# Optimization experiments

Measured on AMD Instinct MI355X. Metric: run time of the kernel, lower is better.

## Reference

```python
import jax, jax.numpy as jnp
import numpy as np
from jax import lax

EPS = 1e-5
K = 3  # DCN kernel size


def _conv(x, w, pad, lhs_dil=(1, 1)):
    return lax.conv_general_dilated(
        x, w, window_strides=(1, 1), padding=((pad, pad), (pad, pad)),
        lhs_dilation=lhs_dil, dimension_numbers=('NCHW', 'OIHW', 'NCHW'))


def _batchnorm(x, gamma, beta):
    # training-mode BN (batch statistics), matching nn.BatchNorm2d in train()
    m = jnp.mean(x, axis=(0, 2, 3), keepdims=True)
    v = jnp.var(x, axis=(0, 2, 3), keepdims=True)
    return (x - m) * lax.rsqrt(v + EPS) * gamma[None, :, None, None] + beta[None, :, None, None]


def _bilinear_sample(x, py, px):
    # x: [B,C,H,W]; py,px: [B,K2,H,W] fractional sample coords (zero-pad outside)
    B, C, H, W = x.shape
    K2 = py.shape[1]
    y0 = jnp.floor(py)
    x0 = jnp.floor(px)
    wy = (py - y0)[:, None]  # [B,1,K2,H,W]
    wx = (px - x0)[:, None]
    xf = x.reshape(B, C, H * W)

    def gather(yi, xi):
        valid = ((yi >= 0) & (yi <= H - 1) & (xi >= 0) & (xi <= W - 1)).astype(x.dtype)
        yc = jnp.clip(yi, 0, H - 1).astype(jnp.int32)
        xc = jnp.clip(xi, 0, W - 1).astype(jnp.int32)
        idx = (yc * W + xc).reshape(B, 1, -1)
        v = jnp.take_along_axis(xf, idx, axis=2).reshape(B, C, K2, H, W)
        return v * valid[:, None]

    v00 = gather(y0, x0)
    v01 = gather(y0, x0 + 1)
    v10 = gather(y0 + 1, x0)
    v11 = gather(y0 + 1, x0 + 1)
    return (v00 * (1 - wy) * (1 - wx) + v01 * (1 - wy) * wx
            + v10 * wy * (1 - wx) + v11 * wy * wx)  # [B,C,K2,H,W]


def _dcn(x, w_off, b_off, w_dcn, b_dcn):
    # Modulated deformable conv (DCNv2), stride 1, pad 1, dil 1, 1 deform group
    B, C, H, W = x.shape
    K2 = K * K
    om = _conv(x, w_off, pad=1) + b_off[None, :, None, None]  # [B,3*K2,H,W]
    dy, dx, m = om[:, :K2], om[:, K2:2 * K2], jax.nn.sigmoid(om[:, 2 * K2:])
    ki, kj = jnp.meshgrid(jnp.arange(K), jnp.arange(K), indexing='ij')
    ky = (ki.reshape(-1) - 1).astype(x.dtype)[None, :, None, None]
    kx = (kj.reshape(-1) - 1).astype(x.dtype)[None, :, None, None]
    py = dy + jnp.arange(H, dtype=x.dtype)[None, None, :, None] + ky
    px = dx + jnp.arange(W, dtype=x.dtype)[None, None, None, :] + kx
    val = _bilinear_sample(x, py, px) * m[:, None]  # [B,C,K2,H,W]
    Co = w_dcn.shape[0]
    out = jnp.einsum('bikhw,oik->bohw', val, w_dcn.reshape(Co, C, K2))
    return out + b_dcn[None, :, None, None]


def _conv_transpose(x, w_up):
    # torch ConvTranspose2d(k=4, stride=2, pad=1), weight [Cin, Cout, 4, 4]
    w = jnp.flip(w_up, axis=(2, 3)).transpose(1, 0, 2, 3)  # -> OIHW
    return _conv(x, w, pad=2, lhs_dil=(2, 2))


def setup_inputs() -> dict:
    key = jax.random.key(0)
    ks = jax.random.split(key, 8)
    B, Cin, Cout, H, W = 4, 256, 256, 64, 64
    x = jax.random.normal(ks[0], (B, Cin, H, W), dtype=jnp.float32)
    w_off = jax.random.normal(ks[1], (3 * K * K, Cin, K, K), dtype=jnp.float32) * 0.01
    b_off = jnp.zeros((3 * K * K,), dtype=jnp.float32)
    w_dcn = jax.random.normal(ks[2], (Cout, Cin, K, K), dtype=jnp.float32) * (1.0 / np.sqrt(Cin * K * K))
    b_dcn = jnp.zeros((Cout,), dtype=jnp.float32)
    gamma1 = jax.random.uniform(ks[3], (Cout,), dtype=jnp.float32, minval=0.5, maxval=1.5)
    beta1 = jax.random.normal(ks[4], (Cout,), dtype=jnp.float32) * 0.1
    w_up = jax.random.normal(ks[5], (Cout, Cout, 4, 4), dtype=jnp.float32) * (1.0 / np.sqrt(Cout * 16))
    gamma2 = jax.random.uniform(ks[6], (Cout,), dtype=jnp.float32, minval=0.5, maxval=1.5)
    beta2 = jax.random.normal(ks[7], (Cout,), dtype=jnp.float32) * 0.1
    return {'x': x, 'w_off': w_off, 'b_off': b_off, 'w_dcn': w_dcn, 'b_dcn': b_dcn,
            'gamma1': gamma1, 'beta1': beta1, 'w_up': w_up, 'gamma2': gamma2, 'beta2': beta2}


def reference(x, w_off, b_off, w_dcn, b_dcn, gamma1, beta1, w_up, gamma2, beta2):
    out = _dcn(x, w_off, b_off, w_dcn, b_dcn)
    out = jax.nn.relu(_batchnorm(out, gamma1, beta1))
    out = _conv_transpose(out, w_up)
    out = jax.nn.relu(_batchnorm(out, gamma2, beta2))
    return out
```

## Files before the change

### kernel.cpp

```cpp
#include <hip/hip_runtime.h>
#include <hip/hip_bf16.h>
#include <math.h>

#define B_   4
#define CIN  256
#define COUT 256
#define HW   4096

typedef __attribute__((ext_vector_type(8))) short short8;
typedef __attribute__((ext_vector_type(4))) float float4v;

#define LSTR  40
#define LSTR2 72

__device__ __forceinline__ float sigmoidf_(float v){ return 1.0f/(1.0f+expf(-v)); }
__device__ __forceinline__ ushort f2bf(float f){
  union { float f; unsigned u; } x; x.f = f;
  unsigned r = x.u + 0x7fffu + ((x.u>>16)&1u);
  return (ushort)(r>>16);
}
__device__ __forceinline__ float bflo(unsigned u){ union{unsigned u; float f;} c; c.u = u<<16;          return c.f; }
__device__ __forceinline__ float bfhi(unsigned u){ union{unsigned u; float f;} c; c.u = u & 0xffff0000u; return c.f; }

__global__ void k_transpose_x(const float* __restrict__ x, ushort* __restrict__ xtb){
  __shared__ float ts[32][33];
  int tx = threadIdx.x & 31, ty = threadIdx.x >> 5;
  int p0 = blockIdx.x * 32, c0 = blockIdx.y * 32, b = blockIdx.z;
  const float* xb = x + (size_t)b*CIN*HW;
#pragma unroll
  for(int q=0;q<4;q++){
    int c = ty + q*8;
    ts[c][tx] = xb[(size_t)(c0+c)*HW + p0+tx];
  }
  __syncthreads();
#pragma unroll
  for(int q=0;q<4;q++){
    int pr = ty + q*8;
    xtb[((size_t)(b*HW + p0+pr)<<8) + c0+tx] = f2bf(ts[tx][pr]);
  }
}

__global__ void k_build_Wob(const float* __restrict__ w_off, ushort* __restrict__ Wob){
  int f = blockIdx.x*256 + threadIdx.x;
  int kc = f>>10, o = (f>>5)&31, kk = f&31;
  int k = kc*32 + kk, tap = k>>8, c = k&255;
  float v = (o < 27) ? w_off[(size_t)o*2304 + c*9 + tap] : 0.f;
  Wob[f] = f2bf(v);
}
__global__ void k_build_Wdb(const float* __restrict__ w_dcn, ushort* __restrict__ Wdb){
  int f = blockIdx.x*256 + threadIdx.x;
  int kc = f>>13, o = (f>>5)&255, kk = f&31;
  int k = kc>>3, c = ((kc&7)<<5) | kk;
  Wdb[f] = f2bf(w_dcn[(size_t)o*2304 + c*9 + k]);
}
__global__ void k_build_WT2c(const float* __restrict__ w_up, ushort* __restrict__ WT2c){
  int f = blockIdx.x*256 + threadIdx.x;
  int pp = f>>18, kc = (f>>13)&31, o = (f>>5)&255, kk = f&31;
  int k = kc*32 + kk, ab = k>>8, c = k&255;
  int a = ab>>1, bb = ab&1, ph = pp>>1, pw = pp&1;
  WT2c[f] = f2bf(w_up[(size_t)(c*COUT+o)*16 + (3-ph-2*a)*4 + (3-pw-2*bb)]);
}

__global__ __launch_bounds__(256) void k_offset_mfma(const ushort* __restrict__ xtb,
                        const ushort* __restrict__ Wob, float* __restrict__ om){
  __shared__ ushort Vs[2][64*LSTR2];
  __shared__ int sIdx[576];
  int tid = threadIdx.x;
  int px0 = blockIdx.x * 64;
  int b   = blockIdx.y;
  for(int t=tid; t<576; t+=256){
    int tap = t>>6, px = t&63;
    int p = px0+px, hh = p>>6, ww = p&63;
    int ih = hh + tap/3 - 1, iw = ww + tap%3 - 1;
    sIdx[t] = (ih>=0 && ih<64 && iw>=0 && iw<64) ? ((b*HW + ih*64+iw)<<8) : -1;
  }
  __syncthreads();

  int lane = tid&63, wv = tid>>6, lo = lane&15, hi = lane>>4;
  float4v acc[2];
  acc[0] = acc[1] = (float4v){0.f,0.f,0.f,0.f};
  int vpx = tid>>2, vseg = tid&3;
  const int wlane = lo*32 + hi*8;

#define OFF_GATHER_P(PAIR, V0, V1) do{ \
    int k_ = (PAIR)>>2, c0_ = ((PAIR)&3)<<6; \
    int idx_ = sIdx[(k_<<6)+vpx]; \
    int coff_ = c0_ + (vseg<<4); \
    V0 = make_uint4(0,0,0,0); V1 = make_uint4(0,0,0,0); \
    if(idx_ >= 0){ \
      V0 = *(const uint4*)(xtb + idx_ + coff_); \
      V1 = *(const uint4*)(xtb + idx_ + coff_ + 8); \
    } \
  }while(0)

#define OFF_VWRITE_P(V0, V1, BUF) do{ \
    *(uint4*)(&Vs[BUF][vpx*LSTR2 + (vseg<<4)])     = V0; \
    *(uint4*)(&Vs[BUF][vpx*LSTR2 + (vseg<<4) + 8]) = V1; \
  }while(0)

#define OFF_WLOAD_P(PAIR, W) do{ \
    const ushort* wp_ = Wob + (((PAIR)*2)<<10) + wlane; \
    W[0] = *(const short8*)(wp_);        W[1] = *(const short8*)(wp_ + 512); \
    W[2] = *(const short8*)(wp_ + 1024); W[3] = *(const short8*)(wp_ + 1536); \
  }while(0)

#define OFF_COMPUTE_P(W, BUF) do{ \
    const ushort* bp_ = &Vs[BUF][(wv*16+lo)*LSTR2 + hi*8]; \
    short8 ba_ = *(const short8*)(bp_); \
    short8 bb_ = *(const short8*)(bp_ + 32); \
    acc[0] = __builtin_amdgcn_mfma_f32_16x16x32_bf16(W[0], ba_, acc[0], 0,0,0); \
    acc[1] = __builtin_amdgcn_mfma_f32_16x16x32_bf16(W[1], ba_, acc[1], 0,0,0); \
    acc[0] = __builtin_amdgcn_mfma_f32_16x16x32_bf16(W[2], bb_, acc[0], 0,0,0); \
    acc[1] = __builtin_amdgcn_mfma_f32_16x16x32_bf16(W[3], bb_, acc[1], 0,0,0); \
  }while(0)

  short8 wA[4], wB[4];
  uint4 vE0, vE1, vO0, vO1;
  OFF_WLOAD_P(0, wA);
  OFF_GATHER_P(0, vE0, vE1);
  OFF_VWRITE_P(vE0, vE1, 0);
  OFF_GATHER_P(1, vO0, vO1);
  __syncthreads();

#pragma unroll 1
  for(int pb=0; pb<36; pb+=2){
    {
      if(pb<34) OFF_GATHER_P(pb+2, vE0, vE1);
      OFF_WLOAD_P(pb+1, wB);
      OFF_COMPUTE_P(wA, 0);
      OFF_VWRITE_P(vO0, vO1, 1);
      __syncthreads();
    }
    {
      if(pb<33) OFF_GATHER_P(pb+3, vO0, vO1);
      if(pb<34) OFF_WLOAD_P(pb+2, wA);
      OFF_COMPUTE_P(wB, 1);
      if(pb<34) OFF_VWRITE_P(vE0, vE1, 0);
      __syncthreads();
    }
  }
  int p = px0 + wv*16 + lo;
#pragma unroll
  for(int mi=0;mi<2;mi++){
    int ob = mi*16 + hi*4;
    float4v a = (mi==0) ? acc[0] : acc[1];
#pragma unroll
    for(int r=0;r<4;r++){
      int o = ob + r;
      if(o < 27) om[(size_t)(b*27+o)*HW + p] = a[r];
    }
  }
}

#define DCN_GATHER_P(PAIR, C0,C1,C2,C3, CF) do{ \
    int k_ = (PAIR)>>2, c0_ = ((PAIR)&3)<<6; \
    int t_ = (k_<<6) + vpx; \
    int pk_ = sPk[t_]; CF = sCf[t_]; \
    int coff_ = c0_ + (vseg<<3); \
    int iy0_=pk_&63, iy1_=(pk_>>6)&63, ix0_=(pk_>>12)&63, ix1_=(pk_>>18)&63; \
    C0 = *(const uint4*)(xtb + cbase + (((iy0_<<6)+ix0_)<<8) + coff_); \
    C1 = *(const uint4*)(xtb + cbase + (((iy0_<<6)+ix1_)<<8) + coff_); \
    C2 = *(const uint4*)(xtb + cbase + (((iy1_<<6)+ix0_)<<8) + coff_); \
    C3 = *(const uint4*)(xtb + cbase + (((iy1_<<6)+ix1_)<<8) + coff_); \
  }while(0)

#define DCN_BLEND_P(C0,C1,C2,C3, CF, BUF) do{ \
    union{ ushort us[8]; uint4 q; } rr_; \
    rr_.us[0] = f2bf(CF.x*bflo(C0.x)+CF.y*bflo(C1.x)+CF.z*bflo(C2.x)+CF.w*bflo(C3.x)); \
    rr_.us[1] = f2bf(CF.x*bfhi(C0.x)+CF.y*bfhi(C1.x)+CF.z*bfhi(C2.x)+CF.w*bfhi(C3.x)); \
    rr_.us[2] = f2bf(CF.x*bflo(C0.y)+CF.y*bflo(C1.y)+CF.z*bflo(C2.y)+CF.w*bflo(C3.y)); \
    rr_.us[3] = f2bf(CF.x*bfhi(C0.y)+CF.y*bfhi(C1.y)+CF.z*bfhi(C2.y)+CF.w*bfhi(C3.y)); \
    rr_.us[4] = f2bf(CF.x*bflo(C0.z)+CF.y*bflo(C1.z)+CF.z*bflo(C2.z)+CF.w*bflo(C3.z)); \
    rr_.us[5] = f2bf(CF.x*bfhi(C0.z)+CF.y*bfhi(C1.z)+CF.z*bfhi(C2.z)+CF.w*bfhi(C3.z)); \
    rr_.us[6] = f2bf(CF.x*bflo(C0.w)+CF.y*bflo(C1.w)+CF.z*bflo(C2.w)+CF.w*bflo(C3.w)); \
    rr_.us[7] = f2bf(CF.x*bfhi(C0.w)+CF.y*bfhi(C1.w)+CF.z*bfhi(C2.w)+CF.w*bfhi(C3.w)); \
    *(uint4*)(&Vs[BUF][vpx*LSTR2 + (vseg<<3)]) = rr_.q; \
  }while(0)

#define DCN_WLOAD_P(PAIR, W) do{ \
    const ushort* wp_ = Wdb + ((size_t)((PAIR)*2)<<13) + wlane; \
    W[0] = *(const short8*)(wp_);         W[1] = *(const short8*)(wp_ + 512); \
    W[2] = *(const short8*)(wp_ + 1024);  W[3] = *(const short8*)(wp_ + 1536); \
    W[4] = *(const short8*)(wp_ + 8192);  W[5] = *(const short8*)(wp_ + 8704); \
    W[6] = *(const short8*)(wp_ + 9216);  W[7] = *(const short8*)(wp_ + 9728); \
  }while(0)

#define DCN_COMPUTE_P(W, BUF) do{ \
    const ushort* bp_ = &Vs[BUF][(pn0+lo)*LSTR2 + hi*8]; \
    short8 a0_ = *(const short8*)(bp_); \
    short8 a1_ = *(const short8*)(bp_ + 16*LSTR2); \
    short8 b0_ = *(const short8*)(bp_ + 32); \
    short8 b1_ = *(const short8*)(bp_ + 32 + 16*LSTR2); \
    _Pragma("unroll") \
    for(int i_=0;i_<4;i_++){ \
      acc[i_][0] = __builtin_amdgcn_mfma_f32_16x16x32_bf16(W[i_],   a0_, acc[i_][0], 0,0,0); \
      acc[i_][1] = __builtin_amdgcn_mfma_f32_16x16x32_bf16(W[i_],   a1_, acc[i_][1], 0,0,0); \
      acc[i_][0] = __builtin_amdgcn_mfma_f32_16x16x32_bf16(W[4+i_], b0_, acc[i_][0], 0,0,0); \
      acc[i_][1] = __builtin_amdgcn_mfma_f32_16x16x32_bf16(W[4+i_], b1_, acc[i_][1], 0,0,0); \
    } \
  }while(0)

__global__ __launch_bounds__(512) void k_dcn_mfma(const ushort* __restrict__ xtb,
                        const float* __restrict__ om, const float* __restrict__ b_off,
                        const ushort* __restrict__ Wdb, float* __restrict__ out1){
  __shared__ ushort Vs[2][64*LSTR2];
  __shared__ int    sPk[576];
  __shared__ float4 sCf[576];
  int tid = threadIdx.x;
  int px0 = blockIdx.x * 64;
  int b   = blockIdx.y;

  for(int t=tid; t<576; t+=512){
    int k = t>>6, px = t&63;
    int p = px0 + px, hh = p>>6, ww = p&63;
    const float* omp = om + (size_t)b*27*HW + p;
    float dy = omp[(size_t)k*HW]      + b_off[k];
    float dx = omp[(size_t)(9+k)*HW]  + b_off[9+k];
    float mo = sigmoidf_(omp[(size_t)(18+k)*HW] + b_off[18+k]);
    float py  = dy + (float)(hh + k/3 - 1);
    float pxf = dx + (float)(ww + k%3 - 1);
    float y0 = floorf(py), x0 = floorf(pxf);
    float wy = py - y0, wx = pxf - x0;
    float y1 = y0 + 1.0f, x1 = x0 + 1.0f;
    bool vy0 = (y0>=0.f)&&(y0<=63.f), vy1 = (y1>=0.f)&&(y1<=63.f);
    bool vx0 = (x0>=0.f)&&(x0<=63.f), vx1 = (x1>=0.f)&&(x1<=63.f);
    int iy0 = (int)fminf(fmaxf(y0,0.f),63.f);
    int iy1 = (int)fminf(fmaxf(y1,0.f),63.f);
    int ix0 = (int)fminf(fmaxf(x0,0.f),63.f);
    int ix1 = (int)fminf(fmaxf(x1,0.f),63.f);
    sPk[t] = iy0 | (iy1<<6) | (ix0<<12) | (ix1<<18);
    sCf[t] = make_float4((vy0&&vx0)? (1.f-wy)*(1.f-wx)*mo : 0.f,
                         (vy0&&vx1)? (1.f-wy)*wx*mo       : 0.f,
                         (vy1&&vx0)? wy*(1.f-wx)*mo       : 0.f,
                         (vy1&&vx1)? wy*wx*mo             : 0.f);
  }
  __syncthreads();

  int lane = tid&63, wv = tid>>6, lo = lane&15, hi = lane>>4;
  int om0 = (wv>>1)*64, pn0 = (wv&1)*32;
  float4v acc[4][2];
#pragma unroll
  for(int i=0;i<4;i++)
#pragma unroll
    for(int j=0;j<2;j++) acc[i][j] = (float4v){0.f,0.f,0.f,0.f};
  int cbase = (b*HW)<<8;
  int vpx = tid>>3, vseg = tid&7;
  const int wlane = (om0+lo)*32 + hi*8;

  short8 wA[8], wB[8];
  uint4 cE0,cE1,cE2,cE3, cO0,cO1,cO2,cO3;
  float4 fE, fO;

  DCN_WLOAD_P(0, wA);
  DCN_GATHER_P(0, cE0,cE1,cE2,cE3, fE);
  DCN_BLEND_P(cE0,cE1,cE2,cE3, fE, 0);
  DCN_GATHER_P(1, cO0,cO1,cO2,cO3, fO);
  __syncthreads();

#pragma unroll 1
  for(int pb=0; pb<36; pb+=2){
    {
      if(pb<34) DCN_GATHER_P(pb+2, cE0,cE1,cE2,cE3, fE);
      DCN_WLOAD_P(pb+1, wB);
      DCN_COMPUTE_P(wA, 0);
      DCN_BLEND_P(cO0,cO1,cO2,cO3, fO, 1);
      __syncthreads();
    }
    {
      if(pb<33) DCN_GATHER_P(pb+3, cO0,cO1,cO2,cO3, fO);
      if(pb<34) DCN_WLOAD_P(pb+2, wA);
      DCN_COMPUTE_P(wB, 1);
      if(pb<34) DCN_BLEND_P(cE0,cE1,cE2,cE3, fE, 0);
      __syncthreads();
    }
  }

#pragma unroll
  for(int i=0;i<4;i++){
    int ob = om0 + i*16 + hi*4;
#pragma unroll
    for(int r=0;r<4;r++){
      int o = ob + r;
      float* op = out1 + (size_t)(b*COUT + o)*HW + px0 + pn0 + lo;
#pragma unroll
      for(int j=0;j<2;j++) op[j*16] = acc[i][j][r];
    }
  }
}

__global__ void k_bn_stats(const float* __restrict__ xin, float* __restrict__ stats, int per_b){
  int o = blockIdx.x, tid = threadIdx.x;
  float s=0.f, ss=0.f;
  for(int b=0;b<B_;b++){
    const float* p = xin + (size_t)(b*COUT+o)*per_b;
    for(int i=tid;i<per_b;i+=256){ float v = p[i]; s+=v; ss+=v*v; }
  }
  __shared__ float rs[256], rss[256];
  rs[tid]=s; rss[tid]=ss; __syncthreads();
  for(int st=128; st>0; st>>=1){
    if(tid<st){ rs[tid]+=rs[tid+st]; rss[tid]+=rss[tid+st]; }
    __syncthreads();
  }
  if(tid==0){
    float n = (float)(B_*per_b);
    float mean = rs[0]/n;
    float var  = rss[0]/n - mean*mean;
    stats[o*2] = mean; stats[o*2+1] = rsqrtf(var + 1e-5f);
  }
}

__global__ void k_bn_stats_ct(const ushort* __restrict__ ct, float* __restrict__ stats){
  int o = blockIdx.x, tid = threadIdx.x;
  float s=0.f, ss=0.f;
  for(int pl=0; pl<16; ++pl){
    const ushort* p = ct + (((size_t)(pl*256 + o))<<12);
    for(int i=tid*8; i<4096; i+=2048){
      uint4 v = *(const uint4*)(p + i);
      float f;
      f=bflo(v.x); s+=f; ss+=f*f;  f=bfhi(v.x); s+=f; ss+=f*f;
      f=bflo(v.y); s+=f; ss+=f*f;  f=bfhi(v.y); s+=f; ss+=f*f;
      f=bflo(v.z); s+=f; ss+=f*f;  f=bfhi(v.z); s+=f; ss+=f*f;
      f=bflo(v.w); s+=f; ss+=f*f;  f=bfhi(v.w); s+=f; ss+=f*f;
    }
  }
  __shared__ float rs[256], rss[256];
  rs[tid]=s; rss[tid]=ss; __syncthreads();
  for(int st=128; st>0; st>>=1){
    if(tid<st){ rs[tid]+=rs[tid+st]; rss[tid]+=rss[tid+st]; }
    __syncthreads();
  }
  if(tid==0){
    float n = (float)(16*4096);
    float mean = rs[0]/n;
    float var  = rss[0]/n - mean*mean;
    stats[o*2] = mean; stats[o*2+1] = rsqrtf(var + 1e-5f);
  }
}

__global__ void k_bn1_apply_t(const float* __restrict__ out1, const float* __restrict__ stats,
                              const float* __restrict__ gamma, const float* __restrict__ beta,
                              ushort* __restrict__ y1b){
  __shared__ float ts[32][33];
  int tx = threadIdx.x & 31, ty = threadIdx.x >> 5;
  int p0 = blockIdx.x*32, o0 = blockIdx.y*32, b = blockIdx.z;
#pragma unroll
  for(int q=0;q<4;q++){
    int oo = ty + q*8; int o = o0 + oo;
    float m = stats[o*2], rstd = stats[o*2+1];
    float scale = rstd * gamma[o];
    float shift = beta[o] - m * scale;
    float v = out1[(size_t)(b*COUT+o)*HW + p0+tx];
    ts[oo][tx] = fmaxf(v*scale + shift, 0.f);
  }
  __syncthreads();
#pragma unroll
  for(int q=0;q<4;q++){
    int pr = ty + q*8;
    y1b[((size_t)(b*HW + p0+pr)<<8) + o0+tx] = f2bf(ts[tx][pr]);
  }
}

__global__ __launch_bounds__(512) void k_convt_mfma(const ushort* __restrict__ y1b,
                        const ushort* __restrict__ WT2c,
                        ushort* __restrict__ ct){
  __shared__ ushort Ws[2][256*LSTR];
  __shared__ ushort Vs[2][256*LSTR];
  __shared__ int sIdx[1024];
  int tid = threadIdx.x;
  int px0 = blockIdx.x * 256;
  int b   = blockIdx.y;
  int pp  = blockIdx.z;
  int ph = pp>>1, pw = pp&1;

  for(int t=tid; t<1024; t+=512){
    int ab = t>>8, px = t&255;
    int a = ab>>1, bb = ab&1;
    int p = px0+px, r = p>>6, s = p&63;
    int ih = r + ph - 1 + a, iw = s + pw - 1 + bb;
    sIdx[t] = (ih>=0 && ih<64 && iw>=0 && iw<64) ? ((b*HW + ih*64+iw)<<8) : -1;
  }
  __syncthreads();

  int lane = tid&63, wv = tid>>6, lo = lane&15, hi = lane>>4;
  int om0 = (wv>>1)*64;
  int pn0 = (wv&1)*128;
  float4v acc[4][8];
#pragma unroll
  for(int i=0;i<4;i++)
#pragma unroll
    for(int j=0;j<8;j++) acc[i][j] = (float4v){0.f,0.f,0.f,0.f};

  const ushort* wbase = WT2c + ((size_t)pp<<18);
  uint4 wpre[2], vpre[2];
  int g1 = tid + 512;
  int vpx = tid>>1, co = (tid&1)*16;

#define CT_PREFETCH(KN) do{ \
    const ushort* wp_ = wbase + ((KN)<<13); \
    wpre[0] = *(const uint4*)(wp_ + tid*8); \
    wpre[1] = *(const uint4*)(wp_ + g1*8); \
    int ab_ = (KN)>>3, c0_ = ((KN)&7)<<5; \
    int idx_ = sIdx[(ab_<<8) + vpx]; \
    int co_ = c0_ + co; \
    vpre[0] = make_uint4(0,0,0,0); vpre[1] = make_uint4(0,0,0,0); \
    if(idx_ >= 0){ \
      vpre[0] = *(const uint4*)(y1b + idx_ + co_); \
      vpre[1] = *(const uint4*)(y1b + idx_ + co_ + 8); \
    } \
  }while(0)

#define CT_WRITE(BUF) do{ \
    *(uint4*)(&Ws[BUF][(tid>>2)*LSTR + (tid&3)*8]) = wpre[0]; \
    *(uint4*)(&Ws[BUF][(g1>>2)*LSTR + (g1&3)*8])   = wpre[1]; \
    *(uint4*)(&Vs[BUF][vpx*LSTR + co])     = vpre[0]; \
    *(uint4*)(&Vs[BUF][vpx*LSTR + co + 8]) = vpre[1]; \
  }while(0)

  CT_PREFETCH(0);
  CT_WRITE(0);
  __syncthreads();

#pragma unroll 1
  for(int kc=0; kc<32; ++kc){
    int cur = kc&1;
    if(kc < 31) CT_PREFETCH(kc+1);
    const ushort* ap = &Ws[cur][(om0 + lo)*LSTR + hi*8];
    const ushort* bp = &Vs[cur][(pn0 + lo)*LSTR + hi*8];
    short8 bfr[8];
#pragma unroll
    for(int j=0;j<8;j++) bfr[j] = *(const short8*)(bp + j*16*LSTR);
#pragma unroll
    for(int i=0;i<4;i++){
      short8 afr = *(const short8*)(ap + i*16*LSTR);
#pragma unroll
      for(int j=0;j<8;j++)
        acc[i][j] = __builtin_amdgcn_mfma_f32_16x16x32_bf16(afr, bfr[j], acc[i][j], 0,0,0);
    }
    if(kc < 31) CT_WRITE(cur^1);
    __syncthreads();
  }

  ushort* cb = ct + (((size_t)(pp*4 + b)*256)<<12);
#pragma unroll
  for(int i=0;i<4;i++){
#pragma unroll
    for(int r=0;r<4;r++){
      int o = om0 + i*16 + hi*4 + r;
      ushort* row = cb + ((size_t)o<<12) + px0 + pn0 + lo;
#pragma unroll
      for(int j=0;j<8;j++) row[j*16] = f2bf(acc[i][j][r]);
    }
  }
}

__global__ void k_bn2_apply(const ushort* __restrict__ ct, const float* __restrict__ stats,
                            const float* __restrict__ gamma, const float* __restrict__ beta,
                            float* __restrict__ out){
  int gid = blockIdx.x*256 + threadIdx.x;
  int e4 = gid<<2;
  int b = e4>>22, o = (e4>>14)&255, q = e4&16383;
  int H2 = q>>7, W2 = q&127;
  int r = H2>>1, ph = H2&1, s0 = W2>>1;
  size_t base0 = (((size_t)((ph*2)*4 + b)*256 + o)<<12) + r*64 + s0;
  unsigned u0 = *(const unsigned*)(ct + base0);
  unsigned u1 = *(const unsigned*)(ct + base0 + ((size_t)4<<20));
  float m = stats[o*2], rstd = stats[o*2+1];
  float sc = rstd * gamma[o];
  float sh = beta[o] - m * sc;
  float4 v;
  v.x = fmaxf(bflo(u0)*sc + sh, 0.f);
  v.y = fmaxf(bflo(u1)*sc + sh, 0.f);
  v.z = fmaxf(bfhi(u0)*sc + sh, 0.f);
  v.w = fmaxf(bfhi(u1)*sc + sh, 0.f);
  *(float4*)(out + e4) = v;
}

extern "C" void kernel_launch(void* const* d_in, const int* in_sizes, int n_in,
                              void* d_out, int out_size, void* d_ws, size_t ws_size,
                              hipStream_t stream){
  (void)in_sizes; (void)n_in; (void)out_size; (void)ws_size;
  const float* x     = (const float*)d_in[0];
  const float* w_off = (const float*)d_in[1];
  const float* b_off = (const float*)d_in[2];
  const float* w_dcn = (const float*)d_in[3];
  const float* gamma1= (const float*)d_in[5];
  const float* beta1 = (const float*)d_in[6];
  const float* w_up  = (const float*)d_in[7];
  const float* gamma2= (const float*)d_in[8];
  const float* beta2 = (const float*)d_in[9];
  float* out = (float*)d_out;

  float* ws   = (float*)d_ws;
  ushort* ct  = (ushort*)ws;
  float* om   = ws;
  ushort* xtb = (ushort*)(ws + 442368);
  float* out1 = ws + 442368 + 2097152;
  float* base2 = ws + 8388608;
  ushort* y1b  = (ushort*)base2;
  ushort* WT2c = (ushort*)(base2 + 2097152);
  ushort* Wdb  = (ushort*)(base2 + 2097152 + 524288);
  ushort* Wob  = (ushort*)(base2 + 2097152 + 524288 + 294912);
  float* st1   = base2 + 2097152 + 524288 + 294912 + 36864;
  float* st2   = st1 + 512;

  k_transpose_x <<<dim3(128,8,4), 256, 0, stream>>>(x, xtb);
  k_build_Wob   <<<288,  256, 0, stream>>>(w_off, Wob);
  k_build_Wdb   <<<2304, 256, 0, stream>>>(w_dcn, Wdb);
  k_build_WT2c  <<<4096, 256, 0, stream>>>(w_up, WT2c);
  k_offset_mfma <<<dim3(64,4),  256, 0, stream>>>(xtb, Wob, om);
  k_dcn_mfma    <<<dim3(64,4),  512, 0, stream>>>(xtb, om, b_off, Wdb, out1);
  k_bn_stats    <<<256,  256, 0, stream>>>(out1, st1, 4096);
  k_bn1_apply_t <<<dim3(128,8,4), 256, 0, stream>>>(out1, st1, gamma1, beta1, y1b);
  k_convt_mfma  <<<dim3(16,4,4),  512, 0, stream>>>(y1b, WT2c, ct);
  k_bn_stats_ct <<<256,  256, 0, stream>>>(ct, st2);
  k_bn2_apply   <<<16384,256, 0, stream>>>(ct, st2, gamma2, beta2, out);
}
```

Before: 289.1 us.

## Restructure transposed-conv GEMM: smaller pixel tiles, direct-from-global weight fragments, K=64 stages

```diff
diff --git a/kernel.cpp b/kernel.cpp
--- a/kernel.cpp
+++ b/kernel.cpp
@@ -360,20 +360,19 @@
   }
 }
 
-__global__ __launch_bounds__(512) void k_convt_mfma(const ushort* __restrict__ y1b,
+__global__ __launch_bounds__(256) void k_convt_mfma(const ushort* __restrict__ y1b,
                         const ushort* __restrict__ WT2c,
                         ushort* __restrict__ ct){
-  __shared__ ushort Ws[2][256*LSTR];
-  __shared__ ushort Vs[2][256*LSTR];
-  __shared__ int sIdx[1024];
+  __shared__ ushort Vs[2][128*LSTR2];
+  __shared__ int sIdx[512];
   int tid = threadIdx.x;
-  int px0 = blockIdx.x * 256;
+  int px0 = blockIdx.x * 128;
   int b   = blockIdx.y;
   int pp  = blockIdx.z;
   int ph = pp>>1, pw = pp&1;
 
-  for(int t=tid; t<1024; t+=512){
-    int ab = t>>8, px = t&255;
+  for(int t=tid; t<512; t+=256){
+    int ab = t>>7, px = t&127;
     int a = ab>>1, bb = ab&1;
     int p = px0+px, r = p>>6, s = p&63;
     int ih = r + ph - 1 + a, iw = s + pw - 1 + bb;
@@ -382,8 +381,7 @@
   __syncthreads();
 
   int lane = tid&63, wv = tid>>6, lo = lane&15, hi = lane>>4;
-  int om0 = (wv>>1)*64;
-  int pn0 = (wv&1)*128;
+  int om0 = wv*64;
   float4v acc[4][8];
 #pragma unroll
   for(int i=0;i<4;i++)
@@ -391,52 +389,57 @@
     for(int j=0;j<8;j++) acc[i][j] = (float4v){0.f,0.f,0.f,0.f};
 
   const ushort* wbase = WT2c + ((size_t)pp<<18);
-  uint4 wpre[2], vpre[2];
-  int g1 = tid + 512;
-  int vpx = tid>>1, co = (tid&1)*16;
-
-#define CT_PREFETCH(KN) do{ \
-    const ushort* wp_ = wbase + ((KN)<<13); \
-    wpre[0] = *(const uint4*)(wp_ + tid*8); \
-    wpre[1] = *(const uint4*)(wp_ + g1*8); \
-    int ab_ = (KN)>>3, c0_ = ((KN)&7)<<5; \
-    int idx_ = sIdx[(ab_<<8) + vpx]; \
-    int co_ = c0_ + co; \
-    vpre[0] = make_uint4(0,0,0,0); vpre[1] = make_uint4(0,0,0,0); \
+  const int wlane = (om0+lo)*32 + hi*8;
+  int vpx = tid>>1, vseg = tid&1;
+  uint4 vpre[4];
+
+#define CT2_PREFETCH(PC) do{ \
+    int kc0_ = (PC)*2; \
+    int ab_ = kc0_>>3, c0_ = (kc0_&7)<<5; \
+    int idx_ = sIdx[(ab_<<7) + vpx]; \
+    int co_ = c0_ + vseg*32; \
+    vpre[0]=make_uint4(0,0,0,0); vpre[1]=make_uint4(0,0,0,0); \
+    vpre[2]=make_uint4(0,0,0,0); vpre[3]=make_uint4(0,0,0,0); \
     if(idx_ >= 0){ \
       vpre[0] = *(const uint4*)(y1b + idx_ + co_); \
       vpre[1] = *(const uint4*)(y1b + idx_ + co_ + 8); \
+      vpre[2] = *(const uint4*)(y1b + idx_ + co_ + 16); \
+      vpre[3] = *(const uint4*)(y1b + idx_ + co_ + 24); \
     } \
   }while(0)
 
-#define CT_WRITE(BUF) do{ \
-    *(uint4*)(&Ws[BUF][(tid>>2)*LSTR + (tid&3)*8]) = wpre[0]; \
-    *(uint4*)(&Ws[BUF][(g1>>2)*LSTR + (g1&3)*8])   = wpre[1]; \
-    *(uint4*)(&Vs[BUF][vpx*LSTR + co])     = vpre[0]; \
-    *(uint4*)(&Vs[BUF][vpx*LSTR + co + 8]) = vpre[1]; \
-  }while(0)
-
-  CT_PREFETCH(0);
-  CT_WRITE(0);
+#define CT2_WRITE(BUF) do{ \
+    ushort* vp_ = &Vs[BUF][vpx*LSTR2 + vseg*32]; \
+    *(uint4*)(vp_)      = vpre[0]; \
+    *(uint4*)(vp_ + 8)  = vpre[1]; \
+    *(uint4*)(vp_ + 16) = vpre[2]; \
+    *(uint4*)(vp_ + 24) = vpre[3]; \
+  }while(0)
+
+  CT2_PREFETCH(0);
+  CT2_WRITE(0);
   __syncthreads();
 
 #pragma unroll 1
-  for(int kc=0; kc<32; ++kc){
-    int cur = kc&1;
-    if(kc < 31) CT_PREFETCH(kc+1);
-    const ushort* ap = &Ws[cur][(om0 + lo)*LSTR + hi*8];
-    const ushort* bp = &Vs[cur][(pn0 + lo)*LSTR + hi*8];
-    short8 bfr[8];
-#pragma unroll
-    for(int j=0;j<8;j++) bfr[j] = *(const short8*)(bp + j*16*LSTR);
-#pragma unroll
-    for(int i=0;i<4;i++){
-      short8 afr = *(const short8*)(ap + i*16*LSTR);
-#pragma unroll
-      for(int j=0;j<8;j++)
-        acc[i][j] = __builtin_amdgcn_mfma_f32_16x16x32_bf16(afr, bfr[j], acc[i][j], 0,0,0);
-    }
-    if(kc < 31) CT_WRITE(cur^1);
+  for(int pc=0; pc<16; ++pc){
+    int cur = pc&1;
+    if(pc < 15) CT2_PREFETCH(pc+1);
+#pragma unroll
+    for(int c=0; c<2; ++c){
+      const ushort* bp = &Vs[cur][lo*LSTR2 + c*32 + hi*8];
+      short8 bfr[8];
+#pragma unroll
+      for(int j=0;j<8;j++) bfr[j] = *(const short8*)(bp + j*16*LSTR2);
+      const ushort* wp = wbase + (((pc<<1)|c)<<13) + wlane;
+#pragma unroll
+      for(int i=0;i<4;i++){
+        short8 afr = *(const short8*)(wp + i*512);
+#pragma unroll
+        for(int j=0;j<8;j++)
+          acc[i][j] = __builtin_amdgcn_mfma_f32_16x16x32_bf16(afr, bfr[j], acc[i][j], 0,0,0);
+      }
+    }
+    if(pc < 15) CT2_WRITE(cur^1);
     __syncthreads();
   }
 
@@ -446,7 +449,7 @@
 #pragma unroll
     for(int r=0;r<4;r++){
       int o = om0 + i*16 + hi*4 + r;
-      ushort* row = cb + ((size_t)o<<12) + px0 + pn0 + lo;
+      ushort* row = cb + ((size_t)o<<12) + px0 + lo;
 #pragma unroll
       for(int j=0;j<8;j++) row[j*16] = f2bf(acc[i][j][r]);
     }
@@ -511,7 +514,7 @@
   k_dcn_mfma    <<<dim3(64,4),  512, 0, stream>>>(xtb, om, b_off, Wdb, out1);
   k_bn_stats    <<<256,  256, 0, stream>>>(out1, st1, 4096);
   k_bn1_apply_t <<<dim3(128,8,4), 256, 0, stream>>>(out1, st1, gamma1, beta1, y1b);
-  k_convt_mfma  <<<dim3(16,4,4),  512, 0, stream>>>(y1b, WT2c, ct);
+  k_convt_mfma  <<<dim3(32,4,4),  256, 0, stream>>>(y1b, WT2c, ct);
   k_bn_stats_ct <<<256,  256, 0, stream>>>(ct, st2);
   k_bn2_apply   <<<16384,256, 0, stream>>>(ct, st2, gamma2, beta2, out);
 }
```

After: 302.7 us. +4.7%, slower.
